# Kernel tuning notes

Hardware: AMD Instinct MI355X
Metric: run time of the kernel (lower is better)

The kernel has to match this reference:

```python
import jax, jax.numpy as jnp
import numpy as np
import math

BATCH, LEN, HID, STATE = 16, 4096, 512, 128
DT_MIN, DT_MAX = 1e-3, 0.1
STEP_RESCALE = 1.0
CONJ_SYM = True


def setup_inputs() -> dict:
    key = jax.random.key(0)
    ks = jax.random.split(key, 7)
    inputs = jax.random.normal(ks[0], (BATCH, LEN, HID), jnp.float32)
    # stable continuous-time eigenvalues: negative real part
    lambda_real = -0.5 * jnp.abs(jax.random.normal(ks[1], (STATE,), jnp.float32)) - 1e-3
    lambda_imag = jnp.pi * jax.random.normal(ks[2], (STATE,), jnp.float32)
    B = jax.random.normal(ks[3], (STATE, HID, 2), jnp.float32) * (1.0 / math.sqrt(HID))
    C = jax.random.normal(ks[4], (HID, STATE, 2), jnp.float32) * (1.0 / math.sqrt(STATE))
    D = jax.random.normal(ks[5], (HID,), jnp.float32)
    u = jax.random.uniform(ks[6], (STATE, 1), jnp.float32)
    log_step = u * (math.log(DT_MAX) - math.log(DT_MIN)) + math.log(DT_MIN)
    return dict(inputs=inputs, lambda_real=lambda_real, lambda_imag=lambda_imag,
                B=B, C=C, D=D, log_step=log_step)


def _s5_forward(inputs, lambda_real, lambda_imag, B, C, D, log_step):
    # complex diagonal state matrix (P,)
    lam = (lambda_real + 1j * lambda_imag).astype(jnp.complex64)
    step = STEP_RESCALE * jnp.exp(log_step[:, 0])          # (P,)
    lambda_bar = jnp.exp(lam * step.astype(jnp.complex64))  # ZOH discretization, (P,)
    B_c = (B[..., 0] + 1j * B[..., 1]).astype(jnp.complex64)  # (P, H)
    C_c = (C[..., 0] + 1j * C[..., 1]).astype(jnp.complex64)  # (H, P)
    # ZOH input matrix: B_bar = (lambda_bar - 1) / lambda * B
    b_bar = ((lambda_bar - 1.0) / lam)[:, None] * B_c          # (P, H)
    # per-timestep driving term: (L, B, P)
    bu = jnp.einsum('blh,ph->lbp', inputs.astype(jnp.complex64), b_bar)
    L = inputs.shape[1]
    a = jnp.broadcast_to(lambda_bar[None, None, :], (L, 1, STATE))  # constant decay per step

    def combine(e1, e2):
        a1, b1 = e1
        a2, b2 = e2
        return (a2 * a1, a2 * b1 + b2)

    # parallel (Blelchoch-style) scan of x_t = lambda_bar * x_{t-1} + bu_t
    _, states = jax.lax.associative_scan(combine, (a, bu))      # states: (L, B, P)
    y = jnp.einsum('lbp,hp->blh', states, C_c)                  # (B, L, H) complex
    out = 2.0 * y.real if CONJ_SYM else y.real
    return out + D * inputs


def reference(inputs, lambda_real, lambda_imag, B, C, D, log_step):
    return _s5_forward(inputs, lambda_real, lambda_imag, B, C, D, log_step)
```

## Files before the change

kernel.cpp:

```cpp
#include <hip/hip_runtime.h>
#include <math.h>

#define B_   16
#define L_   4096
#define H_   512
#define P_   128
#define M_   (B_*L_)
#define N2_  (2*P_)

typedef __attribute__((ext_vector_type(8))) short bf16x8;
typedef __attribute__((ext_vector_type(8))) unsigned short u16x8;
typedef __attribute__((ext_vector_type(4))) float f32x4;
typedef __attribute__((ext_vector_type(4))) unsigned u32x4;

__device__ __forceinline__ unsigned short f2bf(float x) {
    unsigned u = __float_as_uint(x);
    return (unsigned short)((u + 0x7FFFu + ((u >> 16) & 1u)) >> 16);
}
__device__ __forceinline__ float bf2f(unsigned short s) {
    return __uint_as_float(((unsigned)s) << 16);
}
__device__ __forceinline__ unsigned cvtpk(float lo, float hi) {
    unsigned r;
    asm("v_cvt_pk_bf16_f32 %0, %1, %2" : "=v"(r) : "v"(lo), "v"(hi));
    return r;
}

__device__ __forceinline__ void gload16(const void* g, void* l) {
    __builtin_amdgcn_global_load_lds(
        (const __attribute__((address_space(1))) void*)g,
        (__attribute__((address_space(3))) void*)l,
        16, 0, 0);
}


__global__ void precompA(const float* __restrict__ lr, const float* __restrict__ li,
                         const float* __restrict__ lstep,
                         float* __restrict__ abar_r, float* __restrict__ abar_i,
                         float* __restrict__ coef_r, float* __restrict__ coef_i) {
    int p = threadIdx.x;
    if (p >= P_) return;
    double lrd = (double)lr[p], lid = (double)li[p];
    double step = exp((double)lstep[p]);
    double ea = exp(lrd * step);
    double abr = ea * cos(lid * step), abi = ea * sin(lid * step);
    abar_r[p] = (float)abr; abar_i[p] = (float)abi;
    double nr = abr - 1.0, ni = abi;
    double den = lrd*lrd + lid*lid;
    coef_r[p] = (float)((nr*lrd + ni*lid) / den);
    coef_i[p] = (float)((ni*lrd - nr*lid) / den);
}

__global__ void precompBT(const float* __restrict__ Bin,
                          const float* __restrict__ coef_r, const float* __restrict__ coef_i,
                          unsigned short* __restrict__ BTh) {
    int idx = blockIdx.x * 256 + threadIdx.x;
    if (idx >= N2_*H_) return;
    int n = idx >> 9, k = idx & 511;
    int p = n & (P_-1);
    float br = Bin[(p*H_ + k)*2 + 0], bi = Bin[(p*H_ + k)*2 + 1];
    float cr = coef_r[p], ci = coef_i[p];
    float v = (n < P_) ? (cr*br - ci*bi) : (cr*bi + ci*br);
    BTh[idx] = f2bf(v);
}

__global__ void precompCM(const float* __restrict__ Cin,
                          unsigned short* __restrict__ CMh) {
    int idx = blockIdx.x * 256 + threadIdx.x;
    if (idx >= H_*N2_) return;
    int n = idx >> 8, k = idx & 255;
    float v;
    if (k < P_) v =  2.0f * Cin[(n*P_ + k)*2 + 0];
    else        v = -2.0f * Cin[(n*P_ + (k-P_))*2 + 1];
    CMh[idx] = f2bf(v);
}


template<int KSTEPS>
__global__ __launch_bounds__(512) void gemm1f(
        const float* __restrict__ A,
        const unsigned short* __restrict__ Bm,
        unsigned short* __restrict__ bu) {
    constexpr int K = KSTEPS * 64;
    __shared__ float Asf[128 * 64];
    __shared__ unsigned short Bs[256 * 64];

    int t = threadIdx.x;
    int g = blockIdx.x;
    int nid = (g & 7) * (gridDim.x >> 3) + (g >> 3);
    int m0 = nid * 128;

    int lane = t & 63;
    int w    = t >> 6;
    int wr = w >> 2, wc = w & 3;
    int lr = lane & 15, lg = lane >> 4;

    int ar_ = t >> 4;
    int asw = (t & 15) ^ (ar_ & 15);
    const float* gA = A + (size_t)(m0 + ar_) * K + asw * 4;
    int br_ = t >> 3;
    int bsw = (t & 7) ^ (br_ & 7);
    const unsigned short* gB = Bm + (size_t)br_ * K + bsw * 8;

    f32x4 acc[4][4] = {};

    for (int ks = 0; ks < KSTEPS; ++ks) {
        int k0 = ks * 64;
        __syncthreads();
#pragma unroll
        for (int i = 0; i < 4; ++i)
            gload16(gA + (size_t)(32 * i) * K + k0, &Asf[i * 2048 + w * 256]);
#pragma unroll
        for (int i = 0; i < 4; ++i)
            gload16(gB + (size_t)(64 * i) * K + k0, &Bs[i * 4096 + w * 512]);
        __syncthreads();

#pragma unroll
        for (int ku = 0; ku < 2; ++ku) {
            bf16x8 af[4], bf[4];
#pragma unroll
            for (int f = 0; f < 4; ++f) {
                int rA = wr * 64 + f * 16 + lr;
                int c0 = ((ku * 8 + lg * 2)     ^ rA) & 15;
                int c1 = ((ku * 8 + lg * 2 + 1) ^ rA) & 15;
                float4 a0 = *(const float4*)&Asf[rA * 64 + c0 * 4];
                float4 a1 = *(const float4*)&Asf[rA * 64 + c1 * 4];
                u32x4 q;
                q[0] = cvtpk(a0.x, a0.y);
                q[1] = cvtpk(a0.z, a0.w);
                q[2] = cvtpk(a1.x, a1.y);
                q[3] = cvtpk(a1.z, a1.w);
                af[f] = *(bf16x8*)&q;
                int rB = wc * 64 + f * 16 + lr;
                int cb = ((ku * 4 + lg) ^ rB) & 7;
                bf[f] = *(const bf16x8*)&Bs[rB * 64 + cb * 8];
            }
#pragma unroll
            for (int fn = 0; fn < 4; ++fn)
#pragma unroll
                for (int fm = 0; fm < 4; ++fm)
                    acc[fn][fm] = __builtin_amdgcn_mfma_f32_16x16x32_bf16(bf[fn], af[fm], acc[fn][fm], 0, 0, 0);
        }
    }

#pragma unroll
    for (int fn = 0; fn < 4; ++fn)
#pragma unroll
        for (int fm = 0; fm < 4; ++fm) {
            int m = m0 + wr * 64 + fm * 16 + lr;
            int n = wc * 64 + fn * 16 + lg * 4;
            unsigned o0 = cvtpk(acc[fn][fm][0], acc[fn][fm][1]);
            unsigned o1 = cvtpk(acc[fn][fm][2], acc[fn][fm][3]);
            *(uint2*)&bu[(size_t)m * N2_ + n] = make_uint2(o0, o1);
        }
}


template<int KSTEPS, bool HASD>
__global__ __launch_bounds__(256) void gemm_m97(
        const unsigned short* __restrict__ A,
        const unsigned short* __restrict__ Bm,
        float* __restrict__ Cout, int N,
        const float* __restrict__ Din, const float* __restrict__ Dv) {
    constexpr int K = KSTEPS * 64;
    __shared__ unsigned short As[128 * 64];
    __shared__ unsigned short Bs[128 * 64];

    int t = threadIdx.x;
    int nx = gridDim.x;
    int flat = blockIdx.x + nx * blockIdx.y;
    int per  = (nx * gridDim.y) >> 3;
    int nid  = (flat & 7) * per + (flat >> 3);
    int n0 = (nid & (nx - 1)) * 128;
    int m0 = (nid / nx) * 128;

    int lane = t & 63;
    int w    = t >> 6;
    int wr = w >> 1, wc = w & 1;
    int lr = lane & 15, lg = lane >> 4;

    int sr_ = t >> 3;
    int ssw = (t & 7) ^ (sr_ & 7);
    const unsigned short* gA = A  + (size_t)(m0 + sr_) * K + ssw * 8;
    const unsigned short* gB = Bm + (size_t)(n0 + sr_) * K + ssw * 8;

    f32x4 acc[4][4] = {};

    for (int ks = 0; ks < KSTEPS; ++ks) {
        int k0 = ks * 64;
        __syncthreads();
#pragma unroll
        for (int i = 0; i < 4; ++i) {
            gload16(gA + (size_t)(32 * i) * K + k0, &As[i * 2048 + w * 512]);
            gload16(gB + (size_t)(32 * i) * K + k0, &Bs[i * 2048 + w * 512]);
        }
        __syncthreads();

#pragma unroll
        for (int ku = 0; ku < 2; ++ku) {
            bf16x8 af[4], bf[4];
#pragma unroll
            for (int f = 0; f < 4; ++f) {
                int rA = wr * 64 + f * 16 + lr;
                int ca = ((ku * 4 + lg) ^ rA) & 7;
                af[f] = *(const bf16x8*)&As[rA * 64 + ca * 8];
                int rB = wc * 64 + f * 16 + lr;
                int cb = ((ku * 4 + lg) ^ rB) & 7;
                bf[f] = *(const bf16x8*)&Bs[rB * 64 + cb * 8];
            }
#pragma unroll
            for (int fn = 0; fn < 4; ++fn)
#pragma unroll
                for (int fm = 0; fm < 4; ++fm)
                    acc[fn][fm] = __builtin_amdgcn_mfma_f32_16x16x32_bf16(bf[fn], af[fm], acc[fn][fm], 0, 0, 0);
        }
    }

#pragma unroll
    for (int fn = 0; fn < 4; ++fn)
#pragma unroll
        for (int fm = 0; fm < 4; ++fm) {
            int m = m0 + wr * 64 + fm * 16 + lr;
            int n = n0 + wc * 64 + fn * 16 + lg * 4;
            float4 v = make_float4(acc[fn][fm][0], acc[fn][fm][1], acc[fn][fm][2], acc[fn][fm][3]);
            if (HASD) {
                float4 di = *(const float4*)&Din[(size_t)m * N + n];
                float4 dv = *(const float4*)&Dv[n];
                v.x += dv.x * di.x; v.y += dv.y * di.y;
                v.z += dv.z * di.z; v.w += dv.w * di.w;
            }
            *(float4*)&Cout[(size_t)m * N + n] = v;
        }
}


__global__ __launch_bounds__(256) void scan_carry(const unsigned short* __restrict__ bu,
        const float* __restrict__ ar_, const float* __restrict__ ai_,
        float* __restrict__ carr) {
    __shared__ float lds[64][256];
    int t = threadIdx.x;
    int c = blockIdx.x, b = blockIdx.y;
    size_t base = ((size_t)(b*L_ + c*256)) * N2_;
    float ar = 0.f, ai = 0.f, xr = 0.f, xi = 0.f;
    if (t < 128) { ar = ar_[t]; ai = ai_[t]; }
    for (int s = 0; s < 4; s++) {
        __syncthreads();
        const unsigned short* g = bu + base + (size_t)s * 64 * N2_;
#pragma unroll
        for (int it = 0; it < 8; it++) {
            int flat = it * 2048 + t * 8;
            u16x8 v = *(const u16x8*)&g[flat];
            float4 x0 = make_float4(bf2f(v[0]), bf2f(v[1]), bf2f(v[2]), bf2f(v[3]));
            float4 x1 = make_float4(bf2f(v[4]), bf2f(v[5]), bf2f(v[6]), bf2f(v[7]));
            *(float4*)&lds[0][flat]     = x0;
            *(float4*)&lds[0][flat + 4] = x1;
        }
        __syncthreads();
        if (t < 128) {
            for (int i = 0; i < 64; i++) {
                float br = lds[i][t], bi = lds[i][t + 128];
                float nr = ar*xr - ai*xi + br;
                float ni = ar*xi + ai*xr + bi;
                xr = nr; xi = ni;
            }
        }
    }
    if (t < 128) {
        size_t o = ((size_t)(b*16 + c)) * N2_;
        carr[o + t] = xr; carr[o + t + 128] = xi;
    }
}

__global__ void scan_chunks(const float* __restrict__ carr, float* __restrict__ pre,
                            const float* __restrict__ ar_, const float* __restrict__ ai_) {
    int id = blockIdx.x * 256 + threadIdx.x;
    if (id >= B_ * P_) return;
    int b = id >> 7, p = id & (P_-1);
    float mr = ar_[p], mi = ai_[p];
#pragma unroll
    for (int s = 0; s < 8; s++) { float tr = mr*mr - mi*mi; mi = 2.f*mr*mi; mr = tr; }
    float xr = 0.f, xi = 0.f;
    for (int c = 0; c < 16; c++) {
        size_t o = ((size_t)(b*16 + c)) * N2_;
        pre[o + p] = xr; pre[o + p + 128] = xi;
        float cr = carr[o + p], ci = carr[o + p + 128];
        float nr = mr*xr - mi*xi + cr;
        float ni = mr*xi + mi*xr + ci;
        xr = nr; xi = ni;
    }
}

__global__ __launch_bounds__(256) void scan_apply(const unsigned short* __restrict__ bu,
        const float* __restrict__ ar_, const float* __restrict__ ai_,
        const float* __restrict__ pre, unsigned short* __restrict__ states_h) {
    __shared__ float lds[64][256];
    int t = threadIdx.x;
    int c = blockIdx.x, b = blockIdx.y;
    size_t base = ((size_t)(b*L_ + c*256)) * N2_;
    float ar = 0.f, ai = 0.f, xr = 0.f, xi = 0.f;
    if (t < 128) {
        ar = ar_[t]; ai = ai_[t];
        size_t o = ((size_t)(b*16 + c)) * N2_;
        xr = pre[o + t]; xi = pre[o + t + 128];
    }
    for (int s = 0; s < 4; s++) {
        __syncthreads();
        const unsigned short* g = bu + base + (size_t)s * 64 * N2_;
#pragma unroll
        for (int it = 0; it < 8; it++) {
            int flat = it * 2048 + t * 8;
            u16x8 v = *(const u16x8*)&g[flat];
            float4 x0 = make_float4(bf2f(v[0]), bf2f(v[1]), bf2f(v[2]), bf2f(v[3]));
            float4 x1 = make_float4(bf2f(v[4]), bf2f(v[5]), bf2f(v[6]), bf2f(v[7]));
            *(float4*)&lds[0][flat]     = x0;
            *(float4*)&lds[0][flat + 4] = x1;
        }
        __syncthreads();
        if (t < 128) {
            for (int i = 0; i < 64; i++) {
                float br = lds[i][t], bi = lds[i][t + 128];
                float nr = ar*xr - ai*xi + br;
                float ni = ar*xi + ai*xr + bi;
                xr = nr; xi = ni;
                lds[i][t] = xr; lds[i][t + 128] = xi;
            }
        }
        __syncthreads();
        unsigned short* o = states_h + base + (size_t)s * 64 * N2_;
#pragma unroll
        for (int it = 0; it < 8; it++) {
            int flat = it * 2048 + t * 8;
            float4 v0 = *(const float4*)&lds[0][flat];
            float4 v1 = *(const float4*)&lds[0][flat + 4];
            u16x8 ov;
            ov[0] = f2bf(v0.x); ov[1] = f2bf(v0.y); ov[2] = f2bf(v0.z); ov[3] = f2bf(v0.w);
            ov[4] = f2bf(v1.x); ov[5] = f2bf(v1.y); ov[6] = f2bf(v1.z); ov[7] = f2bf(v1.w);
            *(u16x8*)&o[flat] = ov;
        }
    }
}


extern "C" void kernel_launch(void* const* d_in, const int* in_sizes, int n_in,
                              void* d_out, int out_size, void* d_ws, size_t ws_size,
                              hipStream_t stream) {
    const float* inputs = (const float*)d_in[0];
    const float* lr     = (const float*)d_in[1];
    const float* li     = (const float*)d_in[2];
    const float* Bin    = (const float*)d_in[3];
    const float* Cin    = (const float*)d_in[4];
    const float* Dv     = (const float*)d_in[5];
    const float* lstep  = (const float*)d_in[6];
    float* out = (float*)d_out;

    unsigned short* bu = (unsigned short*)d_out;

    float* ws     = (float*)d_ws;
    float* abar_r = ws;
    float* abar_i = ws + 128;
    float* coef_r = ws + 256;
    float* coef_i = ws + 384;
    float* carr   = ws + 512;
    float* pre    = ws + 66048;
    unsigned short* BTh = (unsigned short*)(ws + 131584);
    unsigned short* CMh = BTh + N2_*H_;
    unsigned short* states_h = CMh + H_*N2_;

    hipLaunchKernelGGL(precompA, dim3(1), dim3(128), 0, stream,
                       lr, li, lstep, abar_r, abar_i, coef_r, coef_i);
    hipLaunchKernelGGL(precompBT, dim3((N2_*H_)/256), dim3(256), 0, stream,
                       Bin, coef_r, coef_i, BTh);
    hipLaunchKernelGGL(precompCM, dim3((H_*N2_)/256), dim3(256), 0, stream,
                       Cin, CMh);
    hipLaunchKernelGGL((gemm1f<8>), dim3(M_/128), dim3(512), 0, stream,
                       inputs, BTh, bu);
    hipLaunchKernelGGL(scan_carry, dim3(16, B_), dim3(256), 0, stream,
                       bu, abar_r, abar_i, carr);
    hipLaunchKernelGGL(scan_chunks, dim3(8), dim3(256), 0, stream,
                       carr, pre, abar_r, abar_i);
    hipLaunchKernelGGL(scan_apply, dim3(16, B_), dim3(256), 0, stream,
                       bu, abar_r, abar_i, pre, states_h);
    hipLaunchKernelGGL((gemm_m97<4, true>), dim3(H_/128, M_/128), dim3(256), 0, stream,
                       states_h, CMh, out, H_, inputs, Dv);
}
```

Baseline: 139.6 us.

## Shrink scan chunk to 64 steps to launch more scan blocks

Scan chunks shrink from 256 to 64 timesteps, so scan_carry and scan_apply launch 64x16 = 1024 blocks instead of 256. Each block now loads one tile, scans it and writes once, which removes the inner four-stage loop and its barriers. The serial chunk-combine pass grows from 16 to 64 steps, and the carry and prefix buffers grow, so workspace offsets move. The bf16 store now uses the packed conversion instruction.

```diff
diff --git a/kernel.cpp b/kernel.cpp
--- a/kernel.cpp
+++ b/kernel.cpp
@@ -7,6 +7,8 @@
 #define P_   128
 #define M_   (B_*L_)
 #define N2_  (2*P_)
+#define CHK  64
+#define NCH  (L_/CHK)
 
 typedef __attribute__((ext_vector_type(8))) short bf16x8;
 typedef __attribute__((ext_vector_type(8))) unsigned short u16x8;
@@ -237,36 +239,31 @@
 __global__ __launch_bounds__(256) void scan_carry(const unsigned short* __restrict__ bu,
         const float* __restrict__ ar_, const float* __restrict__ ai_,
         float* __restrict__ carr) {
-    __shared__ float lds[64][256];
+    __shared__ float lds[CHK][256];
     int t = threadIdx.x;
     int c = blockIdx.x, b = blockIdx.y;
-    size_t base = ((size_t)(b*L_ + c*256)) * N2_;
-    float ar = 0.f, ai = 0.f, xr = 0.f, xi = 0.f;
-    if (t < 128) { ar = ar_[t]; ai = ai_[t]; }
-    for (int s = 0; s < 4; s++) {
-        __syncthreads();
-        const unsigned short* g = bu + base + (size_t)s * 64 * N2_;
-#pragma unroll
-        for (int it = 0; it < 8; it++) {
-            int flat = it * 2048 + t * 8;
-            u16x8 v = *(const u16x8*)&g[flat];
-            float4 x0 = make_float4(bf2f(v[0]), bf2f(v[1]), bf2f(v[2]), bf2f(v[3]));
-            float4 x1 = make_float4(bf2f(v[4]), bf2f(v[5]), bf2f(v[6]), bf2f(v[7]));
-            *(float4*)&lds[0][flat]     = x0;
-            *(float4*)&lds[0][flat + 4] = x1;
-        }
-        __syncthreads();
-        if (t < 128) {
-            for (int i = 0; i < 64; i++) {
-                float br = lds[i][t], bi = lds[i][t + 128];
-                float nr = ar*xr - ai*xi + br;
-                float ni = ar*xi + ai*xr + bi;
-                xr = nr; xi = ni;
-            }
-        }
-    }
+    size_t base = ((size_t)(b*L_ + c*CHK)) * N2_;
+    const unsigned short* g = bu + base;
+#pragma unroll
+    for (int it = 0; it < 8; it++) {
+        int flat = it * 2048 + t * 8;
+        u16x8 v = *(const u16x8*)&g[flat];
+        float4 x0 = make_float4(bf2f(v[0]), bf2f(v[1]), bf2f(v[2]), bf2f(v[3]));
+        float4 x1 = make_float4(bf2f(v[4]), bf2f(v[5]), bf2f(v[6]), bf2f(v[7]));
+        *(float4*)&lds[0][flat]     = x0;
+        *(float4*)&lds[0][flat + 4] = x1;
+    }
+    __syncthreads();
     if (t < 128) {
-        size_t o = ((size_t)(b*16 + c)) * N2_;
+        float ar = ar_[t], ai = ai_[t];
+        float xr = 0.f, xi = 0.f;
+        for (int i = 0; i < CHK; i++) {
+            float br = lds[i][t], bi = lds[i][t + 128];
+            float nr = ar*xr - ai*xi + br;
+            float ni = ar*xi + ai*xr + bi;
+            xr = nr; xi = ni;
+        }
+        size_t o = ((size_t)(b*NCH + c)) * N2_;
         carr[o + t] = xr; carr[o + t + 128] = xi;
     }
 }
@@ -278,10 +275,10 @@
     int b = id >> 7, p = id & (P_-1);
     float mr = ar_[p], mi = ai_[p];
 #pragma unroll
-    for (int s = 0; s < 8; s++) { float tr = mr*mr - mi*mi; mi = 2.f*mr*mi; mr = tr; }
+    for (int s = 0; s < 6; s++) { float tr = mr*mr - mi*mi; mi = 2.f*mr*mi; mr = tr; }
     float xr = 0.f, xi = 0.f;
-    for (int c = 0; c < 16; c++) {
-        size_t o = ((size_t)(b*16 + c)) * N2_;
+    for (int c = 0; c < NCH; c++) {
+        size_t o = ((size_t)(b*NCH + c)) * N2_;
         pre[o + p] = xr; pre[o + p + 128] = xi;
         float cr = carr[o + p], ci = carr[o + p + 128];
         float nr = mr*xr - mi*xi + cr;
@@ -293,50 +290,46 @@
 __global__ __launch_bounds__(256) void scan_apply(const unsigned short* __restrict__ bu,
         const float* __restrict__ ar_, const float* __restrict__ ai_,
         const float* __restrict__ pre, unsigned short* __restrict__ states_h) {
-    __shared__ float lds[64][256];
+    __shared__ float lds[CHK][256];
     int t = threadIdx.x;
     int c = blockIdx.x, b = blockIdx.y;
-    size_t base = ((size_t)(b*L_ + c*256)) * N2_;
-    float ar = 0.f, ai = 0.f, xr = 0.f, xi = 0.f;
+    size_t base = ((size_t)(b*L_ + c*CHK)) * N2_;
+    const unsigned short* g = bu + base;
+#pragma unroll
+    for (int it = 0; it < 8; it++) {
+        int flat = it * 2048 + t * 8;
+        u16x8 v = *(const u16x8*)&g[flat];
+        float4 x0 = make_float4(bf2f(v[0]), bf2f(v[1]), bf2f(v[2]), bf2f(v[3]));
+        float4 x1 = make_float4(bf2f(v[4]), bf2f(v[5]), bf2f(v[6]), bf2f(v[7]));
+        *(float4*)&lds[0][flat]     = x0;
+        *(float4*)&lds[0][flat + 4] = x1;
+    }
+    __syncthreads();
     if (t < 128) {
-        ar = ar_[t]; ai = ai_[t];
-        size_t o = ((size_t)(b*16 + c)) * N2_;
-        xr = pre[o + t]; xi = pre[o + t + 128];
-    }
-    for (int s = 0; s < 4; s++) {
-        __syncthreads();
-        const unsigned short* g = bu + base + (size_t)s * 64 * N2_;
-#pragma unroll
-        for (int it = 0; it < 8; it++) {
-            int flat = it * 2048 + t * 8;
-            u16x8 v = *(const u16x8*)&g[flat];
-            float4 x0 = make_float4(bf2f(v[0]), bf2f(v[1]), bf2f(v[2]), bf2f(v[3]));
-            float4 x1 = make_float4(bf2f(v[4]), bf2f(v[5]), bf2f(v[6]), bf2f(v[7]));
-            *(float4*)&lds[0][flat]     = x0;
-            *(float4*)&lds[0][flat + 4] = x1;
-        }
-        __syncthreads();
-        if (t < 128) {
-            for (int i = 0; i < 64; i++) {
-                float br = lds[i][t], bi = lds[i][t + 128];
-                float nr = ar*xr - ai*xi + br;
-                float ni = ar*xi + ai*xr + bi;
-                xr = nr; xi = ni;
-                lds[i][t] = xr; lds[i][t + 128] = xi;
-            }
-        }
-        __syncthreads();
-        unsigned short* o = states_h + base + (size_t)s * 64 * N2_;
-#pragma unroll
-        for (int it = 0; it < 8; it++) {
-            int flat = it * 2048 + t * 8;
-            float4 v0 = *(const float4*)&lds[0][flat];
-            float4 v1 = *(const float4*)&lds[0][flat + 4];
-            u16x8 ov;
-            ov[0] = f2bf(v0.x); ov[1] = f2bf(v0.y); ov[2] = f2bf(v0.z); ov[3] = f2bf(v0.w);
-            ov[4] = f2bf(v1.x); ov[5] = f2bf(v1.y); ov[6] = f2bf(v1.z); ov[7] = f2bf(v1.w);
-            *(u16x8*)&o[flat] = ov;
-        }
+        float ar = ar_[t], ai = ai_[t];
+        size_t o = ((size_t)(b*NCH + c)) * N2_;
+        float xr = pre[o + t], xi = pre[o + t + 128];
+        for (int i = 0; i < CHK; i++) {
+            float br = lds[i][t], bi = lds[i][t + 128];
+            float nr = ar*xr - ai*xi + br;
+            float ni = ar*xi + ai*xr + bi;
+            xr = nr; xi = ni;
+            lds[i][t] = xr; lds[i][t + 128] = xi;
+        }
+    }
+    __syncthreads();
+    unsigned short* o = states_h + base;
+#pragma unroll
+    for (int it = 0; it < 8; it++) {
+        int flat = it * 2048 + t * 8;
+        float4 v0 = *(const float4*)&lds[0][flat];
+        float4 v1 = *(const float4*)&lds[0][flat + 4];
+        unsigned q0 = cvtpk(v0.x, v0.y);
+        unsigned q1 = cvtpk(v0.z, v0.w);
+        unsigned q2 = cvtpk(v1.x, v1.y);
+        unsigned q3 = cvtpk(v1.z, v1.w);
+        u32x4 q = {q0, q1, q2, q3};
+        *(u32x4*)&o[flat] = q;
     }
 }
 
@@ -361,8 +354,8 @@
     float* coef_r = ws + 256;
     float* coef_i = ws + 384;
     float* carr   = ws + 512;
-    float* pre    = ws + 66048;
-    unsigned short* BTh = (unsigned short*)(ws + 131584);
+    float* pre    = ws + 262656;
+    unsigned short* BTh = (unsigned short*)(ws + 524800);
     unsigned short* CMh = BTh + N2_*H_;
     unsigned short* states_h = CMh + H_*N2_;
 
@@ -374,11 +367,11 @@
                        Cin, CMh);
     hipLaunchKernelGGL((gemm1f<8>), dim3(M_/128), dim3(512), 0, stream,
                        inputs, BTh, bu);
-    hipLaunchKernelGGL(scan_carry, dim3(16, B_), dim3(256), 0, stream,
+    hipLaunchKernelGGL(scan_carry, dim3(NCH, B_), dim3(256), 0, stream,
                        bu, abar_r, abar_i, carr);
-    hipLaunchKernelGGL(scan_chunks, dim3(8), dim3(256), 0, stream,
+    hipLaunchKernelGGL(scan_chunks, dim3((B_*P_)/256), dim3(256), 0, stream,
                        carr, pre, abar_r, abar_i);
-    hipLaunchKernelGGL(scan_apply, dim3(16, B_), dim3(256), 0, stream,
+    hipLaunchKernelGGL(scan_apply, dim3(NCH, B_), dim3(256), 0, stream,
                        bu, abar_r, abar_i, pre, states_h);
     hipLaunchKernelGGL((gemm_m97<4, true>), dim3(H_/128, M_/128), dim3(256), 0, stream,
                        states_h, CMh, out, H_, inputs, Dv);
```

Result: no change. 138.0 us (-1.1%).
